# Kernel optimization log

Measured on AMD Instinct MI355X. Metric: run time of the kernel, lower is better.

The kernel has to match this reference:

```python
import jax, jax.numpy as jnp
import numpy as np

D_MODEL = 1024
NUM_HEADS = 16
D_K = D_MODEL // NUM_HEADS


def setup_inputs() -> dict:
    key = jax.random.key(0)
    k1, k2, k3 = jax.random.split(key, 3)
    x = jax.random.normal(k1, (2, 2048, D_MODEL), dtype=jnp.float32)
    # torch Linear(d, 3d): weight shape [3d, d], y = x @ W.T
    W_QKV = jax.random.normal(k2, (3 * D_MODEL, D_MODEL), dtype=jnp.float32) * (1.0 / np.sqrt(D_MODEL))
    W_O = jax.random.normal(k3, (D_MODEL, D_MODEL), dtype=jnp.float32) * (1.0 / np.sqrt(D_MODEL))
    return {"x": x, "W_QKV": W_QKV, "W_O": W_O}


def reference(x, W_QKV, W_O):
    B, T, C = x.shape
    qkv = jnp.einsum('btc,fc->btf', x, W_QKV)  # [B,T,3C]
    q, k, v = jnp.split(qkv, 3, axis=-1)
    def heads(t):
        return t.reshape(B, T, NUM_HEADS, D_K).transpose(0, 2, 1, 3)  # [B,H,T,Dk]
    Q, K, V = heads(q), heads(k), heads(v)
    scores = jnp.einsum('bhqd,bhkd->bhqk', Q, K) / jnp.sqrt(jnp.float32(D_K))
    causal = jnp.tril(jnp.ones((T, T), dtype=bool))
    scores = jnp.where(causal, scores, -jnp.inf)
    attn = jax.nn.softmax(scores, axis=-1)
    out = jnp.einsum('bhqk,bhkd->bhqd', attn, V)
    out = out.transpose(0, 2, 1, 3).reshape(B, T, C)
    return jnp.einsum('btc,oc->bto', out, W_O)
```

## Files before the change

### kernel.cpp

```cpp
#include <hip/hip_runtime.h>
#include <hip/hip_bf16.h>
#include <stdint.h>
#include <stddef.h>


typedef __attribute__((ext_vector_type(8)))  __bf16   bf16x8;
typedef __attribute__((ext_vector_type(4)))  float    f32x4;
typedef __attribute__((ext_vector_type(16))) float    f32x16;
typedef __attribute__((ext_vector_type(4)))  uint32_t u32x4;

#define AS1(p) ((__attribute__((address_space(1))) void*)(p))
#define AS3(p) ((__attribute__((address_space(3))) void*)(p))

static constexpr int Tq    = 2048;
static constexpr int Cd    = 1024;
static constexpr int Mrows = 2 * Tq;

#define QSCALE 0.18033688011112042f

__global__ __launch_bounds__(256) void cvt_bf16_kernel(const float* __restrict__ in,
                                                       __bf16* __restrict__ out, int n8)
{
    int idx    = blockIdx.x * blockDim.x + threadIdx.x;
    int stride = gridDim.x * blockDim.x;
    for (int i = idx; i < n8; i += stride) {
        f32x4 a = ((const f32x4*)in)[i * 2 + 0];
        f32x4 b = ((const f32x4*)in)[i * 2 + 1];
        bf16x8 o;
#pragma unroll
        for (int j = 0; j < 4; ++j) { o[j] = (__bf16)a[j]; o[4 + j] = (__bf16)b[j]; }
        ((bf16x8*)out)[i] = o;
    }
}

__global__ __launch_bounds__(256) void transpose_v_kernel(const __bf16* __restrict__ qkv,
                                                          __bf16* __restrict__ vT)
{
    __shared__ __bf16 tile[64][65];
    const int t   = threadIdx.x;
    const int r0  = blockIdx.x * 64;
    const int hd0 = blockIdx.y * 64;

    {
        const int rr = t >> 2, c16 = (t & 3) * 16;
        const __bf16* src = qkv + (size_t)(r0 + rr) * 3072 + 2048 + hd0 + c16;
        bf16x8 a = *(const bf16x8*)(src);
        bf16x8 b = *(const bf16x8*)(src + 8);
#pragma unroll
        for (int j = 0; j < 8; ++j) { tile[rr][c16 + j] = a[j]; tile[rr][c16 + 8 + j] = b[j]; }
    }
    __syncthreads();
    {
        const int hd_loc = t >> 2, rg = (t & 3) * 16;
        bf16x8 a, b;
#pragma unroll
        for (int j = 0; j < 8; ++j) { a[j] = tile[rg + j][hd_loc]; b[j] = tile[rg + 8 + j][hd_loc]; }
        __bf16* dst = vT + (size_t)(hd0 + hd_loc) * Mrows + r0 + rg;
        *(bf16x8*)(dst)     = a;
        *(bf16x8*)(dst + 8) = b;
    }
}

template <bool OUT_BF16>
__global__ __launch_bounds__(256) void gemm_bt_kernel(const __bf16* __restrict__ A,
                                                      const __bf16* __restrict__ Bm,
                                                      float* __restrict__ Cf,
                                                      __bf16* __restrict__ Cb,
                                                      int N, int K, int qcols, float qscale)
{
    __shared__ __align__(16) __bf16 As[128 * 64];
    __shared__ __align__(16) __bf16 Bs[128 * 64];

    const int tid = threadIdx.x;
    const int l   = tid & 63;
    const int w   = tid >> 6;
    const int wr  = w >> 1, wc = w & 1;
    const int lo  = l & 15, hi = l >> 4;
    const int m0  = blockIdx.x * 128;
    const int n0  = blockIdx.y * 128;

    f32x4 acc[4][4] = {};

    for (int kk = 0; kk < K; kk += 64) {
#pragma unroll
        for (int i = 0; i < 4; ++i) {
            int s   = i * 256 + tid;
            int row = s >> 3;
            int gg  = (s & 7) ^ (row & 7);
            const __bf16* srcA = A  + (size_t)(m0 + row) * K + kk + gg * 8;
            const __bf16* srcB = Bm + (size_t)(n0 + row) * K + kk + gg * 8;
            __builtin_amdgcn_global_load_lds(AS1(srcA), AS3((char*)As + s * 16), 16, 0, 0);
            __builtin_amdgcn_global_load_lds(AS1(srcB), AS3((char*)Bs + s * 16), 16, 0, 0);
        }
        __syncthreads();

#pragma unroll
        for (int ks = 0; ks < 2; ++ks) {
            bf16x8 af[4], bfr[4];
#pragma unroll
            for (int m = 0; m < 4; ++m) {
                int row = wr * 64 + m * 16 + lo;
                int gl  = (ks * 4 + hi) ^ (row & 7);
                af[m] = *(const bf16x8*)((const char*)As + row * 128 + gl * 16);
            }
#pragma unroll
            for (int n = 0; n < 4; ++n) {
                int row = wc * 64 + n * 16 + lo;
                int gl  = (ks * 4 + hi) ^ (row & 7);
                bfr[n] = *(const bf16x8*)((const char*)Bs + row * 128 + gl * 16);
            }
#pragma unroll
            for (int m = 0; m < 4; ++m)
#pragma unroll
                for (int n = 0; n < 4; ++n)
                    acc[m][n] = __builtin_amdgcn_mfma_f32_16x16x32_bf16(af[m], bfr[n], acc[m][n], 0, 0, 0);
        }
        __syncthreads();
    }

#pragma unroll
    for (int m = 0; m < 4; ++m)
#pragma unroll
        for (int n = 0; n < 4; ++n)
#pragma unroll
            for (int r = 0; r < 4; ++r) {
                int row = m0 + wr * 64 + m * 16 + hi * 4 + r;
                int col = n0 + wc * 64 + n * 16 + lo;
                float v = acc[m][n][r];
                if (col < qcols) v *= qscale;
                if (OUT_BF16) Cb[(size_t)row * N + col] = (__bf16)v;
                else          Cf[(size_t)row * N + col] = v;
            }
}

__global__ __launch_bounds__(256) void attn_chunk_kernel(const __bf16* __restrict__ qkv,
                                                         const __bf16* __restrict__ vT,
                                                         __bf16* __restrict__ att,
                                                         __bf16* __restrict__ pO,
                                                         float* __restrict__ stats)
{
    constexpr uint8_t QT[36] = {15,15,15,14,14,14,13,13,13,12,12,12,
                                11,11,11,10, 7, 7, 3,10,10, 9, 9, 6,
                                 6, 9, 8, 8, 8, 5, 5, 2, 4, 4, 1, 0};
    constexpr uint8_t T0[36] = { 0,11,22, 0,10,20, 0,10,19, 0, 9,18,
                                 0, 8,16, 0, 0, 8, 0, 8,15, 0, 7, 0,
                                 7,14, 0, 6,12, 0, 6, 0, 0, 5, 0, 0};
    constexpr uint8_t T1[36] = {11,22,32,10,20,30,10,19,28, 9,18,26,
                                 8,16,24, 8, 8,16, 8,15,22, 7,14, 7,
                                14,20, 6,12,18, 6,12, 6, 5,10, 4, 2};
    constexpr uint8_t SL[36] = {29,30,31,26,27,28,23,24,25,20,21,22,
                                17,18,19,14, 6, 7,255,15,16,11,12, 4,
                                 5,13, 8, 9,10, 2, 3,255, 0, 1,255,255};

    __shared__ __align__(16) __bf16 Ks[2][64 * 64];
    __shared__ __align__(16) __bf16 Vs[2][64 * 64];

    const int tid = threadIdx.x;
    const int l   = tid & 63;
    const int w   = tid >> 6;
    const int lo5 = l & 31, hi5 = l >> 5;

    const int bid = blockIdx.x;
    const int ord = bid >> 5;
    const int bh  = bid & 31;
    const int h   = bh & 15;
    const int b   = bh >> 4;

    const int  qt     = QT[ord];
    const int  sl     = SL[ord];
    const bool direct = (sl == 255);
    const int  t0     = T0[ord];
    const int  t1     = T1[ord];
    const int  qb0    = qt * 128;

    const __bf16* Kbase = qkv + (size_t)b * Tq * 3072 + 1024 + h * 64;
    const __bf16* Vbase = vT  + (size_t)h * 64 * Mrows + b * Tq;

    bf16x8 onesf;
#pragma unroll
    for (int jj = 0; jj < 8; ++jj) onesf[jj] = (__bf16)1.0f;

    const int qg = qb0 + w * 32 + lo5;

    bf16x8 qf[4];
    {
        const __bf16* Qp = qkv + (size_t)(b * Tq + qg) * 3072 + h * 64 + hi5 * 8;
#pragma unroll
        for (int ds = 0; ds < 4; ++ds) qf[ds] = *(const bf16x8*)(Qp + ds * 16);
    }

    f32x16 o0 = {}, o1 = {}, ls = {};
    float m = -1e30f;

#pragma unroll
    for (int i = 0; i < 2; ++i) {
        int s = i * 256 + tid;
        int row = s >> 3, gg = (s & 7) ^ (row & 7);
        __builtin_amdgcn_global_load_lds(AS1(Kbase + (size_t)(t0 * 64 + row) * 3072 + gg * 8),
                                         AS3((char*)Ks[0] + s * 16), 16, 0, 0);
        __builtin_amdgcn_global_load_lds(AS1(Vbase + (size_t)row * Mrows + t0 * 64 + gg * 8),
                                         AS3((char*)Vs[0] + s * 16), 16, 0, 0);
    }
    __syncthreads();

    int cur = 0;
    for (int t = t0; t < t1; ++t) {
        if (t + 1 < t1) {
            const int kn = (t + 1) * 64;
#pragma unroll
            for (int i = 0; i < 2; ++i) {
                int s = i * 256 + tid;
                int row = s >> 3, gg = (s & 7) ^ (row & 7);
                __builtin_amdgcn_global_load_lds(AS1(Kbase + (size_t)(kn + row) * 3072 + gg * 8),
                                                 AS3((char*)Ks[cur ^ 1] + s * 16), 16, 0, 0);
                __builtin_amdgcn_global_load_lds(AS1(Vbase + (size_t)row * Mrows + kn + gg * 8),
                                                 AS3((char*)Vs[cur ^ 1] + s * 16), 16, 0, 0);
            }
        }

        f32x16 sf0 = {}, sf1 = {};
        __builtin_amdgcn_s_setprio(1);
#pragma unroll
        for (int ds = 0; ds < 4; ++ds) {
            {
                int row = lo5;
                int gl  = (ds * 2 + hi5) ^ (row & 7);
                bf16x8 kf = *(const bf16x8*)((const char*)Ks[cur] + row * 128 + gl * 16);
                sf0 = __builtin_amdgcn_mfma_f32_32x32x16_bf16(kf, qf[ds], sf0, 0, 0, 0);
            }
            {
                int row = 32 + lo5;
                int gl  = (ds * 2 + hi5) ^ (row & 7);
                bf16x8 kf = *(const bf16x8*)((const char*)Ks[cur] + row * 128 + gl * 16);
                sf1 = __builtin_amdgcn_mfma_f32_32x32x16_bf16(kf, qf[ds], sf1, 0, 0, 0);
            }
        }
        __builtin_amdgcn_s_setprio(0);

        if (t * 64 + 63 > qb0 + w * 32) {
#pragma unroll
            for (int r = 0; r < 16; ++r) {
                int kcg = t * 64 + (r & 3) + 8 * (r >> 2) + 4 * hi5;
                if (kcg      > qg) sf0[r] = -1e30f;
                if (kcg + 32 > qg) sf1[r] = -1e30f;
            }
        }

        float t0m = fmaxf(sf0[0],  fmaxf(sf0[1],  sf0[2]));
        float t1m = fmaxf(sf0[3],  fmaxf(sf0[4],  sf0[5]));
        float t2m = fmaxf(sf0[6],  fmaxf(sf0[7],  sf0[8]));
        float t3m = fmaxf(sf0[9],  fmaxf(sf0[10], sf0[11]));
        float t4m = fmaxf(sf0[12], fmaxf(sf0[13], sf0[14]));
        float t5m = fmaxf(sf1[0],  fmaxf(sf1[1],  sf1[2]));
        float t6m = fmaxf(sf1[3],  fmaxf(sf1[4],  sf1[5]));
        float t7m = fmaxf(sf1[6],  fmaxf(sf1[7],  sf1[8]));
        float t8m = fmaxf(sf1[9],  fmaxf(sf1[10], sf1[11]));
        float t9m = fmaxf(sf1[12], fmaxf(sf1[13], sf1[14]));
        float u0 = fmaxf(t0m, fmaxf(t1m, t2m));
        float u1 = fmaxf(t3m, fmaxf(t4m, sf0[15]));
        float u2 = fmaxf(t5m, fmaxf(t6m, t7m));
        float u3 = fmaxf(t8m, fmaxf(t9m, sf1[15]));
        float pmh = fmaxf(fmaxf(u0, u1), fmaxf(u2, u3));
        float pm  = fmaxf(pmh, __shfl_xor(pmh, 32));

        if (__any(pm > m + 8.0f)) {
            float mnew = fmaxf(m, pm);
            float fac  = __builtin_amdgcn_exp2f(m - mnew);
            m = mnew;
#pragma unroll
            for (int r = 0; r < 16; ++r) {
                int qreg = (r & 3) + 8 * (r >> 2) + 4 * hi5;
                float fr = __shfl(fac, qreg);
                o0[r] *= fr;
                o1[r] *= fr;
                ls[r] *= fr;
            }
        }

        __builtin_amdgcn_s_setprio(1);
#pragma unroll
        for (int kb = 0; kb < 2; ++kb) {
            uint32_t W[8];
#pragma unroll
            for (int wd = 0; wd < 8; ++wd) {
                float sa = (kb == 0) ? sf0[2 * wd]     : sf1[2 * wd];
                float sb = (kb == 0) ? sf0[2 * wd + 1] : sf1[2 * wd + 1];
                __bf16 ba = (__bf16)__builtin_amdgcn_exp2f(sa - m);
                __bf16 bb = (__bf16)__builtin_amdgcn_exp2f(sb - m);
                W[wd] = (uint32_t)__builtin_bit_cast(uint16_t, ba)
                      | ((uint32_t)__builtin_bit_cast(uint16_t, bb) << 16);
            }
            uint32_t Za = __shfl_xor(hi5 ? W[0] : W[2], 32);
            uint32_t Zb = __shfl_xor(hi5 ? W[1] : W[3], 32);
            uint32_t Zc = __shfl_xor(hi5 ? W[4] : W[6], 32);
            uint32_t Zd = __shfl_xor(hi5 ? W[5] : W[7], 32);

            {
                u32x4 fw = { hi5 ? Za : W[0], hi5 ? Zb : W[1],
                             hi5 ? W[2] : Za, hi5 ? W[3] : Zb };
                bf16x8 pa = __builtin_bit_cast(bf16x8, fw);
                const int kstep = kb * 2;
                {
                    int row = lo5;
                    int gl  = (kstep * 2 + hi5) ^ (row & 7);
                    bf16x8 vb = *(const bf16x8*)((const char*)Vs[cur] + row * 128 + gl * 16);
                    o0 = __builtin_amdgcn_mfma_f32_32x32x16_bf16(pa, vb, o0, 0, 0, 0);
                }
                {
                    int row = 32 + lo5;
                    int gl  = (kstep * 2 + hi5) ^ (row & 7);
                    bf16x8 vb = *(const bf16x8*)((const char*)Vs[cur] + row * 128 + gl * 16);
                    o1 = __builtin_amdgcn_mfma_f32_32x32x16_bf16(pa, vb, o1, 0, 0, 0);
                }
                ls = __builtin_amdgcn_mfma_f32_32x32x16_bf16(pa, onesf, ls, 0, 0, 0);
            }
            {
                u32x4 fw = { hi5 ? Zc : W[4], hi5 ? Zd : W[5],
                             hi5 ? W[6] : Zc, hi5 ? W[7] : Zd };
                bf16x8 pa = __builtin_bit_cast(bf16x8, fw);
                const int kstep = kb * 2 + 1;
                {
                    int row = lo5;
                    int gl  = (kstep * 2 + hi5) ^ (row & 7);
                    bf16x8 vb = *(const bf16x8*)((const char*)Vs[cur] + row * 128 + gl * 16);
                    o0 = __builtin_amdgcn_mfma_f32_32x32x16_bf16(pa, vb, o0, 0, 0, 0);
                }
                {
                    int row = 32 + lo5;
                    int gl  = (kstep * 2 + hi5) ^ (row & 7);
                    bf16x8 vb = *(const bf16x8*)((const char*)Vs[cur] + row * 128 + gl * 16);
                    o1 = __builtin_amdgcn_mfma_f32_32x32x16_bf16(pa, vb, o1, 0, 0, 0);
                }
                ls = __builtin_amdgcn_mfma_f32_32x32x16_bf16(pa, onesf, ls, 0, 0, 0);
            }
        }
        __builtin_amdgcn_s_setprio(0);

        __syncthreads();
        cur ^= 1;
    }

    if (direct) {
#pragma unroll
        for (int r = 0; r < 16; ++r) {
            float lr   = __builtin_amdgcn_rcpf(ls[r]);
            int   qreg = (r & 3) + 8 * (r >> 2) + 4 * hi5;
            int   rowg = b * Tq + qb0 + w * 32 + qreg;
            att[(size_t)rowg * Cd + h * 64 + lo5]      = (__bf16)(o0[r] * lr);
            att[(size_t)rowg * Cd + h * 64 + 32 + lo5] = (__bf16)(o1[r] * lr);
        }
    } else {
        const int slot = bh * 32 + sl;
        __bf16* po = pO + (size_t)slot * 8192;
#pragma unroll
        for (int r = 0; r < 16; ++r) {
            float lr   = __builtin_amdgcn_rcpf(ls[r]);
            int   qreg = (r & 3) + 8 * (r >> 2) + 4 * hi5;
            int   row  = w * 32 + qreg;
            po[row * 64 + lo5]      = (__bf16)(o0[r] * lr);
            po[row * 64 + 32 + lo5] = (__bf16)(o1[r] * lr);
            float mq = __shfl(m, qreg);
            if (lo5 == 0)
                stats[(size_t)slot * 128 + row] = mq + __builtin_amdgcn_logf(ls[r]);
        }
    }
}

__global__ __launch_bounds__(256) void attn_merge_kernel(const __bf16* __restrict__ pO,
                                                         const float* __restrict__ stats,
                                                         __bf16* __restrict__ att)
{
    const int mo  = blockIdx.x;
    const int bh  = mo & 31;
    const int qq  = mo >> 5;
    const int qt  = 4 + qq;
    const int h   = bh & 15;
    const int b   = bh >> 4;

    const int ncc   = (qt >= 8) ? 3 : 2;
    const int slot0 = bh * 32 + ((qt < 8) ? (qt - 4) * 2 : 8 + (qt - 8) * 3);

    const int tid = threadIdx.x;
    const int row = tid >> 1;
    const int c0  = (tid & 1) * 32;

    float L0 = stats[(size_t)(slot0 + 0) * 128 + row];
    float L1 = stats[(size_t)(slot0 + 1) * 128 + row];
    float L2 = (ncc == 3) ? stats[(size_t)(slot0 + 2) * 128 + row] : -1e30f;
    float M  = fmaxf(L0, fmaxf(L1, L2));
    float w0 = __builtin_amdgcn_exp2f(L0 - M);
    float w1 = __builtin_amdgcn_exp2f(L1 - M);
    float w2 = (ncc == 3) ? __builtin_amdgcn_exp2f(L2 - M) : 0.0f;
    float inv = 1.0f / (w0 + w1 + w2);
    w0 *= inv; w1 *= inv; w2 *= inv;

    const __bf16* p0 = pO + (size_t)(slot0 + 0) * 8192 + row * 64 + c0;
    const __bf16* p1 = pO + (size_t)(slot0 + 1) * 8192 + row * 64 + c0;
    const __bf16* p2 = pO + (size_t)(slot0 + 2) * 8192 + row * 64 + c0;

    __bf16* dst = att + (size_t)(b * Tq + qt * 128 + row) * Cd + h * 64 + c0;
#pragma unroll
    for (int i = 0; i < 4; ++i) {
        bf16x8 a = ((const bf16x8*)p0)[i];
        bf16x8 bb = ((const bf16x8*)p1)[i];
        bf16x8 ov;
        if (ncc == 3) {
            bf16x8 cc = ((const bf16x8*)p2)[i];
#pragma unroll
            for (int j = 0; j < 8; ++j)
                ov[j] = (__bf16)(w0 * (float)a[j] + w1 * (float)bb[j] + w2 * (float)cc[j]);
        } else {
#pragma unroll
            for (int j = 0; j < 8; ++j)
                ov[j] = (__bf16)(w0 * (float)a[j] + w1 * (float)bb[j]);
        }
        ((bf16x8*)dst)[i] = ov;
    }
}

extern "C" void kernel_launch(void* const* d_in, const int* in_sizes, int n_in,
                              void* d_out, int out_size, void* d_ws, size_t ws_size,
                              hipStream_t stream)
{
    (void)in_sizes; (void)n_in; (void)out_size; (void)ws_size;

    const float* x    = (const float*)d_in[0];
    const float* Wqkv = (const float*)d_in[1];
    const float* Wo   = (const float*)d_in[2];
    float*       out  = (float*)d_out;

    char* ws = (char*)d_ws;
    __bf16* xb    = (__bf16*)(ws);
    __bf16* wqkvb = (__bf16*)(ws + (size_t)8  * 1024 * 1024);
    __bf16* wob   = (__bf16*)(ws + (size_t)14 * 1024 * 1024);
    __bf16* qkvb  = (__bf16*)(ws + (size_t)16 * 1024 * 1024);
    __bf16* attb  = (__bf16*)(ws + (size_t)40 * 1024 * 1024);
    __bf16* vTb   = xb;
    float*  stats = (float*)wqkvb;
    __bf16* pO    = (__bf16*)out;

    cvt_bf16_kernel<<<2048, 256, 0, stream>>>(x,    xb,    Mrows * Cd / 8);
    cvt_bf16_kernel<<<1536, 256, 0, stream>>>(Wqkv, wqkvb, 3 * Cd * Cd / 8);
    cvt_bf16_kernel<<<512,  256, 0, stream>>>(Wo,   wob,   Cd * Cd / 8);

    dim3 g1(Mrows / 128, 3 * Cd / 128);
    gemm_bt_kernel<true><<<g1, 256, 0, stream>>>(xb, wqkvb, nullptr, qkvb, 3 * Cd, Cd,
                                                 1024, QSCALE);

    dim3 gt(Mrows / 64, Cd / 64);
    transpose_v_kernel<<<gt, 256, 0, stream>>>(qkvb, vTb);

    attn_chunk_kernel<<<1152, 256, 0, stream>>>(qkvb, vTb, attb, pO, stats);
    attn_merge_kernel<<<384, 256, 0, stream>>>(pO, stats, attb);

    dim3 g2(Mrows / 128, Cd / 128);
    gemm_bt_kernel<false><<<g2, 256, 0, stream>>>(attb, wob, out, nullptr, Cd, Cd,
                                                  0, 1.0f);
}
```

Before: 193.8 us.

## Enlarge attention query tile to 256 rows with 512-thread blocks and rebalanced splits

Doubles the attention query tile from 128 to 256 rows, using 8 waves per block so each K/V tile loaded into LDS serves twice as many queries. The split-KV work schedule, partial-output slots and merge kernel are rebuilt for 8 query tiles with up to 3 chunks each. This aims to halve K/V global traffic and LDS fill work per query. In exchange there are fewer blocks (480 instead of 1152), which may leave more of the GPU idle, and load balancing is coarser.

```diff
diff --git a/kernel.cpp b/kernel.cpp
--- a/kernel.cpp
+++ b/kernel.cpp
@@ -133,24 +133,16 @@
             }
 }
 
-__global__ __launch_bounds__(256) void attn_chunk_kernel(const __bf16* __restrict__ qkv,
+__global__ __launch_bounds__(512) void attn_chunk_kernel(const __bf16* __restrict__ qkv,
                                                          const __bf16* __restrict__ vT,
                                                          __bf16* __restrict__ att,
                                                          __bf16* __restrict__ pO,
                                                          float* __restrict__ stats)
 {
-    constexpr uint8_t QT[36] = {15,15,15,14,14,14,13,13,13,12,12,12,
-                                11,11,11,10, 7, 7, 3,10,10, 9, 9, 6,
-                                 6, 9, 8, 8, 8, 5, 5, 2, 4, 4, 1, 0};
-    constexpr uint8_t T0[36] = { 0,11,22, 0,10,20, 0,10,19, 0, 9,18,
-                                 0, 8,16, 0, 0, 8, 0, 8,15, 0, 7, 0,
-                                 7,14, 0, 6,12, 0, 6, 0, 0, 5, 0, 0};
-    constexpr uint8_t T1[36] = {11,22,32,10,20,30,10,19,28, 9,18,26,
-                                 8,16,24, 8, 8,16, 8,15,22, 7,14, 7,
-                                14,20, 6,12,18, 6,12, 6, 5,10, 4, 2};
-    constexpr uint8_t SL[36] = {29,30,31,26,27,28,23,24,25,20,21,22,
-                                17,18,19,14, 6, 7,255,15,16,11,12, 4,
-                                 5,13, 8, 9,10, 2, 3,255, 0, 1,255,255};
+    constexpr uint8_t QT[15] = { 5, 5, 2, 7, 7, 7, 6, 4, 4, 6, 6, 3, 3, 1, 0};
+    constexpr uint8_t T0[15] = { 0,12, 0, 0,11,22, 0, 0,10,10,19, 0, 8, 0, 0};
+    constexpr uint8_t T1[15] = {12,24,12,11,22,32,10,10,20,19,28, 8,16, 8, 4};
+    constexpr uint8_t SL[15] = { 4, 5,255, 9,10,11, 6, 2, 3, 7, 8, 0, 1,255,255};
 
     __shared__ __align__(16) __bf16 Ks[2][64 * 64];
     __shared__ __align__(16) __bf16 Vs[2][64 * 64];
@@ -171,7 +163,7 @@
     const bool direct = (sl == 255);
     const int  t0     = T0[ord];
     const int  t1     = T1[ord];
-    const int  qb0    = qt * 128;
+    const int  qb0    = qt * 256;
 
     const __bf16* Kbase = qkv + (size_t)b * Tq * 3072 + 1024 + h * 64;
     const __bf16* Vbase = vT  + (size_t)h * 64 * Mrows + b * Tq;
@@ -192,14 +184,12 @@
     f32x16 o0 = {}, o1 = {}, ls = {};
     float m = -1e30f;
 
-#pragma unroll
-    for (int i = 0; i < 2; ++i) {
-        int s = i * 256 + tid;
-        int row = s >> 3, gg = (s & 7) ^ (row & 7);
+    {
+        int row = tid >> 3, gg = (tid & 7) ^ (row & 7);
         __builtin_amdgcn_global_load_lds(AS1(Kbase + (size_t)(t0 * 64 + row) * 3072 + gg * 8),
-                                         AS3((char*)Ks[0] + s * 16), 16, 0, 0);
+                                         AS3((char*)Ks[0] + tid * 16), 16, 0, 0);
         __builtin_amdgcn_global_load_lds(AS1(Vbase + (size_t)row * Mrows + t0 * 64 + gg * 8),
-                                         AS3((char*)Vs[0] + s * 16), 16, 0, 0);
+                                         AS3((char*)Vs[0] + tid * 16), 16, 0, 0);
     }
     __syncthreads();
 
@@ -207,15 +197,11 @@
     for (int t = t0; t < t1; ++t) {
         if (t + 1 < t1) {
             const int kn = (t + 1) * 64;
-#pragma unroll
-            for (int i = 0; i < 2; ++i) {
-                int s = i * 256 + tid;
-                int row = s >> 3, gg = (s & 7) ^ (row & 7);
-                __builtin_amdgcn_global_load_lds(AS1(Kbase + (size_t)(kn + row) * 3072 + gg * 8),
-                                                 AS3((char*)Ks[cur ^ 1] + s * 16), 16, 0, 0);
-                __builtin_amdgcn_global_load_lds(AS1(Vbase + (size_t)row * Mrows + kn + gg * 8),
-                                                 AS3((char*)Vs[cur ^ 1] + s * 16), 16, 0, 0);
-            }
+            int row = tid >> 3, gg = (tid & 7) ^ (row & 7);
+            __builtin_amdgcn_global_load_lds(AS1(Kbase + (size_t)(kn + row) * 3072 + gg * 8),
+                                             AS3((char*)Ks[cur ^ 1] + tid * 16), 16, 0, 0);
+            __builtin_amdgcn_global_load_lds(AS1(Vbase + (size_t)row * Mrows + kn + gg * 8),
+                                             AS3((char*)Vs[cur ^ 1] + tid * 16), 16, 0, 0);
         }
 
         f32x16 sf0 = {}, sf1 = {};
@@ -350,8 +336,8 @@
             att[(size_t)rowg * Cd + h * 64 + 32 + lo5] = (__bf16)(o1[r] * lr);
         }
     } else {
-        const int slot = bh * 32 + sl;
-        __bf16* po = pO + (size_t)slot * 8192;
+        const int slot = bh * 12 + sl;
+        __bf16* po = pO + (size_t)slot * 16384;
 #pragma unroll
         for (int r = 0; r < 16; ++r) {
             float lr   = __builtin_amdgcn_rcpf(ls[r]);
@@ -361,7 +347,7 @@
             po[row * 64 + 32 + lo5] = (__bf16)(o1[r] * lr);
             float mq = __shfl(m, qreg);
             if (lo5 == 0)
-                stats[(size_t)slot * 128 + row] = mq + __builtin_amdgcn_logf(ls[r]);
+                stats[(size_t)slot * 256 + row] = mq + __builtin_amdgcn_logf(ls[r]);
         }
     }
 }
@@ -370,23 +356,23 @@
                                                          const float* __restrict__ stats,
                                                          __bf16* __restrict__ att)
 {
+    constexpr uint8_t BASE[5] = {0, 2, 4, 6, 9};
+
     const int mo  = blockIdx.x;
     const int bh  = mo & 31;
-    const int qq  = mo >> 5;
-    const int qt  = 4 + qq;
+    const int qi  = mo >> 5;
+    const int qt  = 3 + qi;
     const int h   = bh & 15;
     const int b   = bh >> 4;
 
-    const int ncc   = (qt >= 8) ? 3 : 2;
-    const int slot0 = bh * 32 + ((qt < 8) ? (qt - 4) * 2 : 8 + (qt - 8) * 3);
-
-    const int tid = threadIdx.x;
-    const int row = tid >> 1;
-    const int c0  = (tid & 1) * 32;
-
-    float L0 = stats[(size_t)(slot0 + 0) * 128 + row];
-    float L1 = stats[(size_t)(slot0 + 1) * 128 + row];
-    float L2 = (ncc == 3) ? stats[(size_t)(slot0 + 2) * 128 + row] : -1e30f;
+    const int ncc   = (qt >= 6) ? 3 : 2;
+    const int slot0 = bh * 12 + BASE[qi];
+
+    const int row = threadIdx.x;
+
+    float L0 = stats[(size_t)(slot0 + 0) * 256 + row];
+    float L1 = stats[(size_t)(slot0 + 1) * 256 + row];
+    float L2 = (ncc == 3) ? stats[(size_t)(slot0 + 2) * 256 + row] : -1e30f;
     float M  = fmaxf(L0, fmaxf(L1, L2));
     float w0 = __builtin_amdgcn_exp2f(L0 - M);
     float w1 = __builtin_amdgcn_exp2f(L1 - M);
@@ -394,14 +380,14 @@
     float inv = 1.0f / (w0 + w1 + w2);
     w0 *= inv; w1 *= inv; w2 *= inv;
 
-    const __bf16* p0 = pO + (size_t)(slot0 + 0) * 8192 + row * 64 + c0;
-    const __bf16* p1 = pO + (size_t)(slot0 + 1) * 8192 + row * 64 + c0;
-    const __bf16* p2 = pO + (size_t)(slot0 + 2) * 8192 + row * 64 + c0;
-
-    __bf16* dst = att + (size_t)(b * Tq + qt * 128 + row) * Cd + h * 64 + c0;
-#pragma unroll
-    for (int i = 0; i < 4; ++i) {
-        bf16x8 a = ((const bf16x8*)p0)[i];
+    const __bf16* p0 = pO + (size_t)(slot0 + 0) * 16384 + row * 64;
+    const __bf16* p1 = pO + (size_t)(slot0 + 1) * 16384 + row * 64;
+    const __bf16* p2 = pO + (size_t)(slot0 + 2) * 16384 + row * 64;
+
+    __bf16* dst = att + (size_t)(b * Tq + qt * 256 + row) * Cd + h * 64;
+#pragma unroll
+    for (int i = 0; i < 8; ++i) {
+        bf16x8 a  = ((const bf16x8*)p0)[i];
         bf16x8 bb = ((const bf16x8*)p1)[i];
         bf16x8 ov;
         if (ncc == 3) {
@@ -450,8 +436,8 @@
     dim3 gt(Mrows / 64, Cd / 64);
     transpose_v_kernel<<<gt, 256, 0, stream>>>(qkvb, vTb);
 
-    attn_chunk_kernel<<<1152, 256, 0, stream>>>(qkvb, vTb, attb, pO, stats);
-    attn_merge_kernel<<<384, 256, 0, stream>>>(pO, stats, attb);
+    attn_chunk_kernel<<<480, 512, 0, stream>>>(qkvb, vTb, attb, pO, stats);
+    attn_merge_kernel<<<160, 256, 0, stream>>>(pO, stats, attb);
 
     dim3 g2(Mrows / 128, Cd / 128);
     gemm_bt_kernel<false><<<g2, 256, 0, stream>>>(attb, wob, out, nullptr, Cd, Cd,
```

Result: no change. 191.5 us (-1.1%).
